# Kernel optimization log

Hardware: AMD Instinct MI355X
Metric: run time of the kernel (lower is better)

## Reference

```python
import jax, jax.numpy as jnp
import numpy as np

N, D = 8192, 1024

def setup_inputs() -> dict:
    key = jax.random.key(0)
    ks = jax.random.split(key, 7)
    s = 1.0 / np.sqrt(D)
    return {
        "sent_mat": jax.random.normal(ks[0], (N, D), dtype=jnp.float32),
        "indicator": 0,
        "Wq": jax.random.normal(ks[1], (D, D), dtype=jnp.float32) * s,
        "bq": jax.random.normal(ks[2], (D,), dtype=jnp.float32) * s,
        "Wk": jax.random.normal(ks[3], (D, D), dtype=jnp.float32) * s,
        "bk": jax.random.normal(ks[4], (D,), dtype=jnp.float32) * s,
        "Wv": jax.random.normal(ks[5], (D, D), dtype=jnp.float32) * s,
        "bv": jax.random.normal(ks[6], (D,), dtype=jnp.float32) * s,
    }

def reference(sent_mat, indicator, Wq, bq, Wk, bk, Wv, bv):
    # torch.nn.Linear: y = x @ W.T + b
    Q = sent_mat @ Wq.T + bq            # [N, D]
    K = sent_mat @ Wk.T + bk            # [N, D]
    V = sent_mat @ Wv.T + bv            # [N, D]
    sim = Q @ K.T                       # [N, N]
    if indicator == 0:                  # custom score inversion
        sim = 1.0 - sim
    sim_norm = sim / jnp.sqrt(jnp.asarray(D, dtype=sim.dtype))
    # NOTE: softmax over dim=0 (columns normalized over rows), unconventional
    attn_w = jax.nn.softmax(sim_norm, axis=0)   # [N, N]
    attn_out = attn_w @ V               # [N, D]
    return (attn_out, attn_w)
```

## Files before the change

kernel.cpp:

```cpp
#include <hip/hip_runtime.h>

#define NT 8192
#define DM 1024

typedef unsigned short u16;
typedef __bf16 bf16x8 __attribute__((ext_vector_type(8)));
typedef float f32x4 __attribute__((ext_vector_type(4)));
typedef u16 u16x8 __attribute__((ext_vector_type(8)));

__device__ __forceinline__ u16 f2bf(float f) {
  union { float f; unsigned u; } v; v.f = f;
  unsigned r = v.u + 0x7fffu + ((v.u >> 16) & 1u);
  return (u16)(r >> 16);
}
__device__ __forceinline__ float bf2f(u16 h) {
  union { unsigned u; float f; } v; v.u = ((unsigned)h) << 16;
  return v.f;
}

__device__ __forceinline__ void stage16(const u16* g, u16* lds_wave_uniform) {
  __builtin_amdgcn_global_load_lds(
      (const __attribute__((address_space(1))) unsigned int*)g,
      (__attribute__((address_space(3))) unsigned int*)lds_wave_uniform, 16, 0, 0);
}

__global__ void cvt_bf16_kernel(const float* __restrict__ in, u16* __restrict__ out, int n4) {
  int i = blockIdx.x * blockDim.x + threadIdx.x;
  int stride = gridDim.x * blockDim.x;
  for (; i < n4; i += stride) {
    float4 v = reinterpret_cast<const float4*>(in)[i];
    ushort4 o;
    o.x = f2bf(v.x); o.y = f2bf(v.y); o.z = f2bf(v.z); o.w = f2bf(v.w);
    reinterpret_cast<ushort4*>(out)[i] = o;
  }
}

__global__ __launch_bounds__(512, 2)
void qkt_exp_256(const u16* __restrict__ Q, const u16* __restrict__ Kmat, int K,
                 u16* __restrict__ E, float* __restrict__ cs,
                 const int* __restrict__ indp) {
  __shared__ u16 AT[2][256 * 64];
  __shared__ u16 BT[2][256 * 64];
  const int t = threadIdx.x;
  const int l = t & 63;
  const int w = t >> 6;
  const int wm = w >> 2;
  const int wn = w & 3;
  const int r16 = l & 15;
  const int half = l >> 4;

  const int gx = gridDim.x;
  const int nwg = gx * gridDim.y;
  int lin = blockIdx.y * gx + blockIdx.x;
  if ((nwg & 7) == 0) lin = (lin & 7) * (nwg >> 3) + (lin >> 3);
  const int bx = lin % gx;
  const int by = lin / gx;
  const size_t brow = (size_t)by * 256;
  const size_t bcol = (size_t)bx * 256;

  const int srow = w * 8 + (l >> 3);
  const int kel = ((l & 7) ^ (l >> 3)) * 8;
  const int ntiles = K >> 6;

  f32x4 acc[8][4] = {};

#pragma unroll
  for (int q = 0; q < 4; ++q) {
    stage16(Q    + (brow + q * 64 + srow) * (size_t)K + kel, &AT[0][q * 4096 + w * 512]);
    stage16(Kmat + (bcol + q * 64 + srow) * (size_t)K + kel, &BT[0][q * 4096 + w * 512]);
  }
  __syncthreads();

  for (int tt = 0; tt < ntiles; ++tt) {
    const int cur = tt & 1;
    const int nxt = cur ^ 1;
    const int k1 = (tt + 1) << 6;
    const bool more = (tt + 1 < ntiles);
#pragma unroll
    for (int p = 0; p < 4; ++p) {
      if (p == 0 && more) {
#pragma unroll
        for (int q = 0; q < 4; ++q)
          stage16(Q + (brow + q * 64 + srow) * (size_t)K + (k1 + kel),
                  &AT[nxt][q * 4096 + w * 512]);
      }
      if (p == 1 && more) {
#pragma unroll
        for (int q = 0; q < 4; ++q)
          stage16(Kmat + (bcol + q * 64 + srow) * (size_t)K + (k1 + kel),
                  &BT[nxt][q * 4096 + w * 512]);
      }
      bf16x8 af[4][2], bfr[2][2];
#pragma unroll
      for (int m = 0; m < 4; ++m) {
        const int row = wm * 128 + (p >> 1) * 64 + m * 16 + r16;
#pragma unroll
        for (int kk = 0; kk < 2; ++kk) {
          const int slot = (half + 4 * kk) ^ (r16 & 7);
          af[m][kk] = *reinterpret_cast<const bf16x8*>(&AT[cur][row * 64 + slot * 8]);
        }
      }
#pragma unroll
      for (int n = 0; n < 2; ++n) {
        const int row = wn * 64 + (p & 1) * 32 + n * 16 + r16;
#pragma unroll
        for (int kk = 0; kk < 2; ++kk) {
          const int slot = (half + 4 * kk) ^ (r16 & 7);
          bfr[n][kk] = *reinterpret_cast<const bf16x8*>(&BT[cur][row * 64 + slot * 8]);
        }
      }
      __builtin_amdgcn_s_setprio(1);
#pragma unroll
      for (int m = 0; m < 4; ++m)
#pragma unroll
        for (int n = 0; n < 2; ++n)
#pragma unroll
          for (int kk = 0; kk < 2; ++kk)
            acc[(p >> 1) * 4 + m][(p & 1) * 2 + n] = __builtin_amdgcn_mfma_f32_16x16x32_bf16(
                af[m][kk], bfr[n][kk], acc[(p >> 1) * 4 + m][(p & 1) * 2 + n], 0, 0, 0);
      __builtin_amdgcn_s_setprio(0);
      __builtin_amdgcn_sched_barrier(0);
    }
    __syncthreads();
  }

  const bool flip = (*indp == 0);
  const float cexp = 0.045084220027780106f;
  float csum[4] = {0.f, 0.f, 0.f, 0.f};
#pragma unroll
  for (int mg = 0; mg < 8; ++mg) {
#pragma unroll
    for (int ng = 0; ng < 4; ++ng) {
#pragma unroll
      for (int q = 0; q < 4; ++q) {
        float s = acc[mg][ng][q];
        float x = flip ? (1.0f - s) : s;
        float e = exp2f(x * cexp);
        size_t row = brow + wm * 128 + mg * 16 + half * 4 + q;
        size_t col = bcol + wn * 64 + ng * 16 + r16;
        E[row * NT + col] = f2bf(e);
        csum[ng] += e;
      }
    }
  }
#pragma unroll
  for (int ng = 0; ng < 4; ++ng) {
    float s = csum[ng];
    s += __shfl_xor(s, 16);
    s += __shfl_xor(s, 32);
    if (l < 16) atomicAdd(&cs[bcol + wn * 64 + ng * 16 + l], s);
  }
}

__global__ __launch_bounds__(512, 2)
void pv_256x128(const u16* __restrict__ A, const u16* __restrict__ B,
                float* __restrict__ C, int K) {
  __shared__ u16 AT[2][256 * 64];
  __shared__ u16 BT[2][128 * 64];
  const int t = threadIdx.x;
  const int l = t & 63;
  const int w = t >> 6;
  const int wm = w >> 2;
  const int wn = w & 3;
  const int r16 = l & 15;
  const int half = l >> 4;

  const int gx = gridDim.x;
  const int nwg = gx * gridDim.y;
  int lin = blockIdx.y * gx + blockIdx.x;
  if ((nwg & 7) == 0) lin = (lin & 7) * (nwg >> 3) + (lin >> 3);
  const int bx = lin % gx;
  const int by = lin / gx;
  const size_t brow = (size_t)by * 256;
  const size_t bcol = (size_t)bx * 128;

  const int srow = w * 8 + (l >> 3);
  const int kel = ((l & 7) ^ (l >> 3)) * 8;
  const int ntiles = K >> 6;

  f32x4 acc[8][2] = {};

#pragma unroll
  for (int q = 0; q < 4; ++q)
    stage16(A + (brow + q * 64 + srow) * (size_t)K + kel, &AT[0][q * 4096 + w * 512]);
#pragma unroll
  for (int q = 0; q < 2; ++q)
    stage16(B + (bcol + q * 64 + srow) * (size_t)K + kel, &BT[0][q * 4096 + w * 512]);
  __syncthreads();

  for (int tt = 0; tt < ntiles; ++tt) {
    const int cur = tt & 1;
    const int nxt = cur ^ 1;
    const int k1 = (tt + 1) << 6;
    const bool more = (tt + 1 < ntiles);
#pragma unroll
    for (int p = 0; p < 2; ++p) {
      if (p == 0 && more) {
#pragma unroll
        for (int q = 0; q < 4; ++q)
          stage16(A + (brow + q * 64 + srow) * (size_t)K + (k1 + kel),
                  &AT[nxt][q * 4096 + w * 512]);
      }
      if (p == 1 && more) {
#pragma unroll
        for (int q = 0; q < 2; ++q)
          stage16(B + (bcol + q * 64 + srow) * (size_t)K + (k1 + kel),
                  &BT[nxt][q * 4096 + w * 512]);
      }
      bf16x8 af[4][2], bfr[2][2];
#pragma unroll
      for (int m = 0; m < 4; ++m) {
        const int row = wm * 128 + p * 64 + m * 16 + r16;
#pragma unroll
        for (int kk = 0; kk < 2; ++kk) {
          const int slot = (half + 4 * kk) ^ (r16 & 7);
          af[m][kk] = *reinterpret_cast<const bf16x8*>(&AT[cur][row * 64 + slot * 8]);
        }
      }
#pragma unroll
      for (int n = 0; n < 2; ++n) {
        const int row = wn * 32 + n * 16 + r16;
#pragma unroll
        for (int kk = 0; kk < 2; ++kk) {
          const int slot = (half + 4 * kk) ^ (r16 & 7);
          bfr[n][kk] = *reinterpret_cast<const bf16x8*>(&BT[cur][row * 64 + slot * 8]);
        }
      }
      __builtin_amdgcn_s_setprio(1);
#pragma unroll
      for (int m = 0; m < 4; ++m)
#pragma unroll
        for (int n = 0; n < 2; ++n)
#pragma unroll
          for (int kk = 0; kk < 2; ++kk)
            acc[p * 4 + m][n] = __builtin_amdgcn_mfma_f32_16x16x32_bf16(
                af[m][kk], bfr[n][kk], acc[p * 4 + m][n], 0, 0, 0);
      __builtin_amdgcn_s_setprio(0);
      __builtin_amdgcn_sched_barrier(0);
    }
    __syncthreads();
  }

#pragma unroll
  for (int mg = 0; mg < 8; ++mg) {
#pragma unroll
    for (int n = 0; n < 2; ++n) {
#pragma unroll
      for (int q = 0; q < 4; ++q) {
        size_t row = brow + wm * 128 + mg * 16 + half * 4 + q;
        size_t col = bcol + wn * 32 + n * 16 + r16;
        C[row * DM + col] = acc[mg][n][q];
      }
    }
  }
}

template<int EPI, int AF32, int BF32>
__global__ __launch_bounds__(256)
void gemm_bt(const void* __restrict__ Av, const void* __restrict__ Bv, int K, int ldo,
             const float* __restrict__ bias, u16* __restrict__ obf,
             float* __restrict__ of32, const int* __restrict__ indp) {
  __shared__ u16 As[128 * 32];
  __shared__ u16 Bs[128 * 32];
  const int t = threadIdx.x;
  const int l = t & 63;
  const int w = t >> 6;
  const int wr = w >> 1;
  const int wc = w & 1;
  const int r16 = l & 15;
  const int half = l >> 4;

  const int gx = gridDim.x;
  const int nwg = gx * gridDim.y;
  int lin = blockIdx.y * gx + blockIdx.x;
  if ((nwg & 7) == 0) lin = (lin & 7) * (nwg >> 3) + (lin >> 3);
  const int bx = lin % gx;
  const int by = lin / gx;

  const size_t brow = (size_t)by * 128;
  const size_t bcol = (size_t)bx * 128;
  const int kel = (l & 3) * 8;
  const int lrow = l >> 2;

  f32x4 acc[4][4] = {};

  for (int k0 = 0; k0 < K; k0 += 32) {
#pragma unroll
    for (int c = 0; c < 2; ++c) {
      const int seg = c * 4 + w;
      const int r = seg * 16 + lrow;
      if constexpr (AF32) {
        const float* ga = (const float*)Av + (brow + r) * (size_t)K + (k0 + kel);
        float4 u0 = *reinterpret_cast<const float4*>(ga);
        float4 u1 = *reinterpret_cast<const float4*>(ga + 4);
        u16x8 o;
        o[0] = f2bf(u0.x); o[1] = f2bf(u0.y); o[2] = f2bf(u0.z); o[3] = f2bf(u0.w);
        o[4] = f2bf(u1.x); o[5] = f2bf(u1.y); o[6] = f2bf(u1.z); o[7] = f2bf(u1.w);
        *reinterpret_cast<u16x8*>(&As[seg * 512 + l * 8]) = o;
      } else {
        const u16* ga = (const u16*)Av + (brow + r) * (size_t)K + (k0 + kel);
        stage16(ga, &As[seg * 512]);
      }
      if constexpr (BF32) {
        const float* gb = (const float*)Bv + (bcol + r) * (size_t)K + (k0 + kel);
        float4 u0 = *reinterpret_cast<const float4*>(gb);
        float4 u1 = *reinterpret_cast<const float4*>(gb + 4);
        u16x8 o;
        o[0] = f2bf(u0.x); o[1] = f2bf(u0.y); o[2] = f2bf(u0.z); o[3] = f2bf(u0.w);
        o[4] = f2bf(u1.x); o[5] = f2bf(u1.y); o[6] = f2bf(u1.z); o[7] = f2bf(u1.w);
        *reinterpret_cast<u16x8*>(&Bs[seg * 512 + l * 8]) = o;
      } else {
        const u16* gb = (const u16*)Bv + (bcol + r) * (size_t)K + (k0 + kel);
        stage16(gb, &Bs[seg * 512]);
      }
    }
    __syncthreads();
    bf16x8 af[4], bfv[4];
#pragma unroll
    for (int m = 0; m < 4; ++m)
      af[m] = *reinterpret_cast<const bf16x8*>(&As[(wr * 64 + m * 16 + r16) * 32 + half * 8]);
#pragma unroll
    for (int n = 0; n < 4; ++n)
      bfv[n] = *reinterpret_cast<const bf16x8*>(&Bs[(wc * 64 + n * 16 + r16) * 32 + half * 8]);
#pragma unroll
    for (int m = 0; m < 4; ++m)
#pragma unroll
      for (int n = 0; n < 4; ++n)
        acc[m][n] = __builtin_amdgcn_mfma_f32_16x16x32_bf16(af[m], bfv[n], acc[m][n], 0, 0, 0);
    __syncthreads();
  }

  const int crow0 = wr * 64 + half * 4;
  const int ccol0 = wc * 64 + r16;

  if constexpr (EPI == 0) {
#pragma unroll
    for (int m = 0; m < 4; ++m) {
#pragma unroll
      for (int n = 0; n < 4; ++n) {
        const int cc = ccol0 + n * 16;
        const float bv = bias[bcol + cc];
#pragma unroll
        for (int q = 0; q < 4; ++q) {
          size_t idx = (brow + crow0 + m * 16 + q) * (size_t)ldo + (bcol + cc);
          obf[idx] = f2bf(acc[m][n][q] + bv);
        }
      }
    }
  } else if constexpr (EPI == 1) {
    const bool flip = (*indp == 0);
    const float cexp = 0.045084220027780106f;
#pragma unroll
    for (int m = 0; m < 4; ++m) {
#pragma unroll
      for (int n = 0; n < 4; ++n) {
        const int cc = ccol0 + n * 16;
#pragma unroll
        for (int q = 0; q < 4; ++q) {
          float s = acc[m][n][q];
          float x = flip ? (1.0f - s) : s;
          size_t idx = (brow + crow0 + m * 16 + q) * (size_t)ldo + (bcol + cc);
          of32[idx] = exp2f(x * cexp);
        }
      }
    }
  } else {
#pragma unroll
    for (int m = 0; m < 4; ++m) {
#pragma unroll
      for (int n = 0; n < 4; ++n) {
        const int cc = ccol0 + n * 16;
#pragma unroll
        for (int q = 0; q < 4; ++q) {
          size_t idx = (brow + crow0 + m * 16 + q) * (size_t)ldo + (bcol + cc);
          of32[idx] = acc[m][n][q];
        }
      }
    }
  }
}

__global__ void colsum_kernel(const float* __restrict__ E, float* __restrict__ cs) {
  const int col = blockIdx.x * 256 + threadIdx.x;
  const int r0 = blockIdx.y * 256;
  float s = 0.f;
  for (int r = r0; r < r0 + 256; ++r)
    s += E[(size_t)r * NT + col];
  atomicAdd(&cs[col], s);
}

__global__ void norm_kernel(float* __restrict__ w, const float* __restrict__ cs, int n4) {
  int i = blockIdx.x * blockDim.x + threadIdx.x;
  int stride = gridDim.x * blockDim.x;
  for (; i < n4; i += stride) {
    float4 v = reinterpret_cast<float4*>(w)[i];
    int j4 = i & (NT / 4 - 1);
    float4 c = reinterpret_cast<const float4*>(cs)[j4];
    v.x /= c.x; v.y /= c.y; v.z /= c.z; v.w /= c.w;
    reinterpret_cast<float4*>(w)[i] = v;
  }
}

__global__ void norm_bf16_kernel(const u16* __restrict__ e, float* __restrict__ w,
                                 const float* __restrict__ cs, int n4) {
  int i = blockIdx.x * blockDim.x + threadIdx.x;
  int stride = gridDim.x * blockDim.x;
  for (; i < n4; i += stride) {
    ushort4 ev = reinterpret_cast<const ushort4*>(e)[i];
    int j4 = i & (NT / 4 - 1);
    float4 c = reinterpret_cast<const float4*>(cs)[j4];
    float4 v;
    v.x = bf2f(ev.x) / c.x;
    v.y = bf2f(ev.y) / c.y;
    v.z = bf2f(ev.z) / c.z;
    v.w = bf2f(ev.w) / c.w;
    reinterpret_cast<float4*>(w)[i] = v;
  }
}

__global__ void vt_kernel(const u16* __restrict__ Vb, const float* __restrict__ cs,
                          u16* __restrict__ Vt) {
  __shared__ u16 tile[64][65];
  const int jb = blockIdx.x * 64;
  const int db = blockIdx.y * 64;
  const int t = threadIdx.x;
  {
    const int d = t & 63;
    const int j0 = t >> 6;
    for (int jj = j0; jj < 64; jj += 4)
      tile[jj][d] = Vb[(size_t)(jb + jj) * DM + db + d];
  }
  __syncthreads();
  {
    const int j = t & 63;
    const int d0 = t >> 6;
    const float inv = cs ? (1.0f / cs[jb + j]) : 1.0f;
    for (int dd = d0; dd < 64; dd += 4) {
      u16 raw = tile[j][dd];
      Vt[(size_t)(db + dd) * NT + jb + j] = cs ? f2bf(bf2f(raw) * inv) : raw;
    }
  }
}

extern "C" void kernel_launch(void* const* d_in, const int* in_sizes, int n_in,
                              void* d_out, int out_size, void* d_ws, size_t ws_size,
                              hipStream_t stream) {
  const float* X  = (const float*)d_in[0];
  const int* indp = (const int*)d_in[1];
  const float* Wq = (const float*)d_in[2];
  const float* bq = (const float*)d_in[3];
  const float* Wk = (const float*)d_in[4];
  const float* bk = (const float*)d_in[5];
  const float* Wv = (const float*)d_in[6];
  const float* bv = (const float*)d_in[7];

  float* attn_out = (float*)d_out;
  float* attn_w   = (float*)d_out + (size_t)NT * DM;

  const size_t EB_BYTES = (size_t)NT * NT * 2;
  const size_t QKV_BYTES = (size_t)NT * DM * 2;
  const size_t need_fast = EB_BYTES + 4 * QKV_BYTES + NT * 4;

  if (ws_size >= need_fast) {
    char* ws = (char*)d_ws;
    u16* Eb = (u16*)ws;
    u16* Qb = (u16*)(ws + EB_BYTES);
    u16* Kb = Qb + (size_t)NT * DM;
    u16* Vb = Kb + (size_t)NT * DM;
    u16* Vt = Vb + (size_t)NT * DM;
    float* cs = (float*)(Vt + (size_t)NT * DM);
    u16* Xb  = Eb;
    u16* Wqb = Eb + (size_t)NT * DM;
    u16* Wkb = Wqb + (size_t)DM * DM;
    u16* Wvb = Wkb + (size_t)DM * DM;

    cvt_bf16_kernel<<<2048, 256, 0, stream>>>(X,  Xb,  NT * DM / 4);
    cvt_bf16_kernel<<<1024, 256, 0, stream>>>(Wq, Wqb, DM * DM / 4);
    cvt_bf16_kernel<<<1024, 256, 0, stream>>>(Wk, Wkb, DM * DM / 4);
    cvt_bf16_kernel<<<1024, 256, 0, stream>>>(Wv, Wvb, DM * DM / 4);

    dim3 gqkv(DM / 128, NT / 128);
    gemm_bt<0, 0, 0><<<gqkv, 256, 0, stream>>>(Xb, Wqb, DM, DM, bq, Qb, nullptr, nullptr);
    gemm_bt<0, 0, 0><<<gqkv, 256, 0, stream>>>(Xb, Wkb, DM, DM, bk, Kb, nullptr, nullptr);
    gemm_bt<0, 0, 0><<<gqkv, 256, 0, stream>>>(Xb, Wvb, DM, DM, bv, Vb, nullptr, nullptr);

    hipMemsetAsync(cs, 0, NT * sizeof(float), stream);
    qkt_exp_256<<<dim3(NT / 256, NT / 256), 512, 0, stream>>>(Qb, Kb, DM, Eb, cs, indp);

    vt_kernel<<<dim3(NT / 64, DM / 64), 256, 0, stream>>>(Vb, cs, Vt);

    pv_256x128<<<dim3(DM / 128, NT / 256), 512, 0, stream>>>(Eb, Vt, attn_out, NT);

    norm_bf16_kernel<<<4096, 256, 0, stream>>>(Eb, attn_w, cs, NT * NT / 4);
  } else {
    char* ws = (char*)d_ws;
    u16* Qb = (u16*)ws;  ws += QKV_BYTES;
    u16* Kb = (u16*)ws;  ws += QKV_BYTES;
    u16* Vb = (u16*)ws;  ws += QKV_BYTES;
    u16* Vt = (u16*)ws;  ws += QKV_BYTES;
    float* cs = (float*)ws;

    dim3 gqkv(DM / 128, NT / 128);
    gemm_bt<0, 1, 1><<<gqkv, 256, 0, stream>>>(X, Wq, DM, DM, bq, Qb, nullptr, nullptr);
    gemm_bt<0, 1, 1><<<gqkv, 256, 0, stream>>>(X, Wk, DM, DM, bk, Kb, nullptr, nullptr);
    gemm_bt<0, 1, 1><<<gqkv, 256, 0, stream>>>(X, Wv, DM, DM, bv, Vb, nullptr, nullptr);

    gemm_bt<1, 0, 0><<<dim3(NT / 128, NT / 128), 256, 0, stream>>>(
        Qb, Kb, DM, NT, nullptr, nullptr, attn_w, indp);

    hipMemsetAsync(cs, 0, NT * sizeof(float), stream);
    colsum_kernel<<<dim3(32, 32), 256, 0, stream>>>(attn_w, cs);
    norm_kernel<<<4096, 256, 0, stream>>>(attn_w, cs, NT * NT / 4);
    vt_kernel<<<dim3(NT / 64, DM / 64), 256, 0, stream>>>(Vb, nullptr, Vt);

    gemm_bt<2, 1, 0><<<dim3(DM / 128, NT / 128), 256, 0, stream>>>(
        attn_w, Vt, NT, DM, nullptr, nullptr, attn_out, nullptr);
  }
}
```

Before: 537.6 us.

## Triple-buffer PV GEMM pipeline and reuse it for QKV projections

Turns the PV kernel into a templated GEMM with three LDS stages, issuing loads two tiles ahead and waiting on a partial vmcnt instead of a full __syncthreads, and hoists B fragment loads out of the inner p loop. The same kernel, with a bias/bf16 epilogue, now replaces the older 128x128 gemm_bt for the Q/K/V projections. The aim is to hide global-load latency and get a larger-tile MFMA kernel for the projections. LDS use grows to 144 KB per block, which may limit occupancy to one block per CU despite the launch bound of 2. The QKV grid also halves to 256 blocks.

```diff
diff --git a/kernel.cpp b/kernel.cpp
--- a/kernel.cpp
+++ b/kernel.cpp
@@ -152,11 +152,14 @@
   }
 }
 
+template<int EPI>
 __global__ __launch_bounds__(512, 2)
-void pv_256x128(const u16* __restrict__ A, const u16* __restrict__ B,
-                float* __restrict__ C, int K) {
-  __shared__ u16 AT[2][256 * 64];
-  __shared__ u16 BT[2][128 * 64];
+void mega_bt(const u16* __restrict__ A, const u16* __restrict__ B, int K, int ldo,
+             const float* __restrict__ bias, u16* __restrict__ obf,
+             float* __restrict__ of32, float* __restrict__ cs,
+             const int* __restrict__ indp) {
+  __shared__ u16 AT[3][256 * 64];
+  __shared__ u16 BT[3][128 * 64];
   const int t = threadIdx.x;
   const int l = t & 63;
   const int w = t >> 6;
@@ -176,38 +179,48 @@
 
   const int srow = w * 8 + (l >> 3);
   const int kel = ((l & 7) ^ (l >> 3)) * 8;
-  const int ntiles = K >> 6;
+  const int nt = K >> 6;
 
   f32x4 acc[8][2] = {};
 
-#pragma unroll
-  for (int q = 0; q < 4; ++q)
-    stage16(A + (brow + q * 64 + srow) * (size_t)K + kel, &AT[0][q * 4096 + w * 512]);
-#pragma unroll
-  for (int q = 0; q < 2; ++q)
-    stage16(B + (bcol + q * 64 + srow) * (size_t)K + kel, &BT[0][q * 4096 + w * 512]);
-  __syncthreads();
-
-  for (int tt = 0; tt < ntiles; ++tt) {
-    const int cur = tt & 1;
-    const int nxt = cur ^ 1;
-    const int k1 = (tt + 1) << 6;
-    const bool more = (tt + 1 < ntiles);
+#define STAGE(tile, buf)                                                              \
+  {                                                                                   \
+    const int k0_ = (tile) << 6;                                                      \
+    _Pragma("unroll")                                                                 \
+    for (int q = 0; q < 4; ++q)                                                       \
+      stage16(A + (brow + q * 64 + srow) * (size_t)K + (k0_ + kel),                   \
+              &AT[buf][q * 4096 + w * 512]);                                          \
+    _Pragma("unroll")                                                                 \
+    for (int q = 0; q < 2; ++q)                                                       \
+      stage16(B + (bcol + q * 64 + srow) * (size_t)K + (k0_ + kel),                   \
+              &BT[buf][q * 4096 + w * 512]);                                          \
+  }
+
+  STAGE(0, 0);
+  STAGE(1, 1);
+
+  for (int tt = 0; tt < nt; ++tt) {
+    const int cur = tt % 3;
+    if (tt < nt - 1) asm volatile("s_waitcnt vmcnt(6)" ::: "memory");
+    else             asm volatile("s_waitcnt vmcnt(0)" ::: "memory");
+    __builtin_amdgcn_s_barrier();
+    __builtin_amdgcn_sched_barrier(0);
+    if (tt + 2 < nt) STAGE(tt + 2, (tt + 2) % 3);
+    __builtin_amdgcn_sched_barrier(0);
+
+    bf16x8 bfr[2][2];
+#pragma unroll
+    for (int n = 0; n < 2; ++n) {
+      const int row = wn * 32 + n * 16 + r16;
+#pragma unroll
+      for (int kk = 0; kk < 2; ++kk) {
+        const int slot = (half + 4 * kk) ^ (r16 & 7);
+        bfr[n][kk] = *reinterpret_cast<const bf16x8*>(&BT[cur][row * 64 + slot * 8]);
+      }
+    }
 #pragma unroll
     for (int p = 0; p < 2; ++p) {
-      if (p == 0 && more) {
-#pragma unroll
-        for (int q = 0; q < 4; ++q)
-          stage16(A + (brow + q * 64 + srow) * (size_t)K + (k1 + kel),
-                  &AT[nxt][q * 4096 + w * 512]);
-      }
-      if (p == 1 && more) {
-#pragma unroll
-        for (int q = 0; q < 2; ++q)
-          stage16(B + (bcol + q * 64 + srow) * (size_t)K + (k1 + kel),
-                  &BT[nxt][q * 4096 + w * 512]);
-      }
-      bf16x8 af[4][2], bfr[2][2];
+      bf16x8 af[4][2];
 #pragma unroll
       for (int m = 0; m < 4; ++m) {
         const int row = wm * 128 + p * 64 + m * 16 + r16;
@@ -215,15 +228,6 @@
         for (int kk = 0; kk < 2; ++kk) {
           const int slot = (half + 4 * kk) ^ (r16 & 7);
           af[m][kk] = *reinterpret_cast<const bf16x8*>(&AT[cur][row * 64 + slot * 8]);
-        }
-      }
-#pragma unroll
-      for (int n = 0; n < 2; ++n) {
-        const int row = wn * 32 + n * 16 + r16;
-#pragma unroll
-        for (int kk = 0; kk < 2; ++kk) {
-          const int slot = (half + 4 * kk) ^ (r16 & 7);
-          bfr[n][kk] = *reinterpret_cast<const bf16x8*>(&BT[cur][row * 64 + slot * 8]);
         }
       }
       __builtin_amdgcn_s_setprio(1);
@@ -238,18 +242,61 @@
       __builtin_amdgcn_s_setprio(0);
       __builtin_amdgcn_sched_barrier(0);
     }
-    __syncthreads();
-  }
-
-#pragma unroll
-  for (int mg = 0; mg < 8; ++mg) {
+  }
+#undef STAGE
+
+  if constexpr (EPI == 0) {
+#pragma unroll
+    for (int mg = 0; mg < 8; ++mg) {
+#pragma unroll
+      for (int n = 0; n < 2; ++n) {
+        const int cc = wn * 32 + n * 16 + r16;
+        const float bv = bias[bcol + cc];
+#pragma unroll
+        for (int q = 0; q < 4; ++q) {
+          size_t row = brow + wm * 128 + mg * 16 + half * 4 + q;
+          obf[row * (size_t)ldo + bcol + cc] = f2bf(acc[mg][n][q] + bv);
+        }
+      }
+    }
+  } else if constexpr (EPI == 1) {
+    const bool flip = (*indp == 0);
+    const float cexp = 0.045084220027780106f;
+    float csum[2] = {0.f, 0.f};
+#pragma unroll
+    for (int mg = 0; mg < 8; ++mg) {
+#pragma unroll
+      for (int n = 0; n < 2; ++n) {
+        const int cc = wn * 32 + n * 16 + r16;
+#pragma unroll
+        for (int q = 0; q < 4; ++q) {
+          float s = acc[mg][n][q];
+          float x = flip ? (1.0f - s) : s;
+          float e = exp2f(x * cexp);
+          size_t row = brow + wm * 128 + mg * 16 + half * 4 + q;
+          obf[row * (size_t)ldo + bcol + cc] = f2bf(e);
+          csum[n] += e;
+        }
+      }
+    }
 #pragma unroll
     for (int n = 0; n < 2; ++n) {
-#pragma unroll
-      for (int q = 0; q < 4; ++q) {
-        size_t row = brow + wm * 128 + mg * 16 + half * 4 + q;
-        size_t col = bcol + wn * 32 + n * 16 + r16;
-        C[row * DM + col] = acc[mg][n][q];
+      float s = csum[n];
+      s += __shfl_xor(s, 16);
+      s += __shfl_xor(s, 32);
+      if (l < 16) atomicAdd(&cs[bcol + wn * 32 + n * 16 + l], s);
+    }
+  } else {
+#pragma unroll
+    for (int mg = 0; mg < 8; ++mg) {
+#pragma unroll
+      for (int n = 0; n < 2; ++n) {
+#pragma unroll
+        for (int q = 0; q < 4; ++q) {
+          size_t row = brow + wm * 128 + mg * 16 + half * 4 + q;
+          size_t col = bcol + wn * 32 + n * 16 + r16;
+          of32[row * (size_t)ldo + col] = acc[mg][n][q];
+        }
       }
     }
   }
@@ -479,17 +526,18 @@
     cvt_bf16_kernel<<<1024, 256, 0, stream>>>(Wk, Wkb, DM * DM / 4);
     cvt_bf16_kernel<<<1024, 256, 0, stream>>>(Wv, Wvb, DM * DM / 4);
 
-    dim3 gqkv(DM / 128, NT / 128);
-    gemm_bt<0, 0, 0><<<gqkv, 256, 0, stream>>>(Xb, Wqb, DM, DM, bq, Qb, nullptr, nullptr);
-    gemm_bt<0, 0, 0><<<gqkv, 256, 0, stream>>>(Xb, Wkb, DM, DM, bk, Kb, nullptr, nullptr);
-    gemm_bt<0, 0, 0><<<gqkv, 256, 0, stream>>>(Xb, Wvb, DM, DM, bv, Vb, nullptr, nullptr);
+    dim3 gqkv(DM / 128, NT / 256);
+    mega_bt<0><<<gqkv, 512, 0, stream>>>(Xb, Wqb, DM, DM, bq, Qb, nullptr, nullptr, nullptr);
+    mega_bt<0><<<gqkv, 512, 0, stream>>>(Xb, Wkb, DM, DM, bk, Kb, nullptr, nullptr, nullptr);
+    mega_bt<0><<<gqkv, 512, 0, stream>>>(Xb, Wvb, DM, DM, bv, Vb, nullptr, nullptr, nullptr);
 
     hipMemsetAsync(cs, 0, NT * sizeof(float), stream);
     qkt_exp_256<<<dim3(NT / 256, NT / 256), 512, 0, stream>>>(Qb, Kb, DM, Eb, cs, indp);
 
     vt_kernel<<<dim3(NT / 64, DM / 64), 256, 0, stream>>>(Vb, cs, Vt);
 
-    pv_256x128<<<dim3(DM / 128, NT / 256), 512, 0, stream>>>(Eb, Vt, attn_out, NT);
+    mega_bt<2><<<dim3(DM / 128, NT / 256), 512, 0, stream>>>(
+        Eb, Vt, NT, DM, nullptr, nullptr, attn_out, nullptr, nullptr);
 
     norm_bf16_kernel<<<4096, 256, 0, stream>>>(Eb, attn_w, cs, NT * NT / 4);
   } else {
```

Result: faster. 512.6 us (-4.7%).
